# Performance work log

Measured on AMD Instinct MI355X. Metric: run time of the kernel, lower is better.

The kernel has to match this reference:

```python
import jax, jax.numpy as jnp
import numpy as np

C_IN = 96          # spectral bands
D2 = 2 * C_IN      # d = 192 (inner dim)
D4 = 4 * D2        # 768 (4-directional scan channels)
N = 16             # SSM state size
DR = 6             # delta_rank = ceil(96/16)
B, H, W = 2, 96, 96  # H,W not in {8,16,32,64} -> s=1 path


def setup_inputs() -> dict:
    key = jax.random.key(0)
    ks = jax.random.split(key, 8)
    g = lambda k, shape, s: jax.random.normal(k, shape, jnp.float32) * s
    return {
        "x": jax.random.normal(ks[0], (B, C_IN, H, W), jnp.float32),
        "W_in": g(ks[1], (C_IN, 2 * D2), 0.05),          # in_proj (in,out)
        "b_in": jnp.zeros((2 * D2,), jnp.float32),
        "w_dw": g(ks[2], (D2, 1, 3, 3), 0.1),            # depthwise conv OIHW
        "b_dw": jnp.zeros((D2,), jnp.float32),
        "A_log": jnp.log(jnp.tile(jnp.arange(1.0, N + 1.0, dtype=jnp.float32), (D4, 1))),
        "Dp": jnp.ones((D4,), jnp.float32),
        "W_x": g(ks[3], (D4, DR + 2 * N), 0.05),         # x_proj, no bias
        "W_delta": g(ks[4], (DR, D4), 0.1),
        "b_delta": g(ks[5], (D4,), 0.1),
        "ln_g": jnp.ones((D2,), jnp.float32),
        "ln_b": jnp.zeros((D2,), jnp.float32),
        "W_out": g(ks[6], (D2, C_IN), 0.05),             # out_proj, no bias
    }


def _selective_scan(u, delta, A, Bm, Cm, Dv):
    # u, delta: [b,L,d4]; Bm, Cm: [b,L,n]; A: [d4,n]; Dv: [d4]
    b, L, d4 = u.shape
    n = A.shape[1]

    def step(h, inps):
        u_t, dt, B_t, C_t = inps                      # [b,d4],[b,d4],[b,n],[b,n]
        dA = jnp.exp(dt[:, :, None] * A)              # [b,d4,n]
        h = dA * h + (dt * u_t)[:, :, None] * B_t[:, None, :]
        y = jnp.einsum('bdn,bn->bd', h, C_t) + Dv * u_t
        return h, y

    h0 = jnp.zeros((b, d4, n), u.dtype)
    xs = (jnp.swapaxes(u, 0, 1), jnp.swapaxes(delta, 0, 1),
          jnp.swapaxes(Bm, 0, 1), jnp.swapaxes(Cm, 0, 1))
    _, ys = jax.lax.scan(step, h0, xs)                # ys: [L,b,d4]
    return jnp.swapaxes(ys, 0, 1)                     # [b,L,d4]


def reference(x, W_in, b_in, w_dw, b_dw, A_log, Dp, W_x, W_delta, b_delta, ln_g, ln_b, W_out):
    b, c, Hh, Ww = x.shape                            # s = 1 (H not in {8,16,32,64})
    d = W_in.shape[1] // 2
    # in_proj on channel-last, chunk into x / gate z
    xz = jnp.einsum('bchw,ce->bhwe', x, W_in) + b_in  # [b,h,w,2d]
    xx, z = jnp.split(xz, 2, axis=-1)
    # depthwise conv + silu
    xc = jnp.transpose(xx, (0, 3, 1, 2))              # [b,d,h,w]
    xc = jax.lax.conv_general_dilated(
        xc, w_dw, (1, 1), 'SAME', feature_group_count=d,
        dimension_numbers=('NCHW', 'OIHW', 'NCHW')) + b_dw[None, :, None, None]
    xc = jax.nn.silu(xc)
    # 4 directional flattenings (with s=1: x1==x2 row-major, x3==x4 reversed)
    L = Hh * Ww
    flat = xc.reshape(b, d, L)
    flipped = xc[:, :, ::-1, ::-1].reshape(b, d, L)
    xl = jnp.swapaxes(jnp.concatenate([flat, flat, flipped, flipped], axis=1), 1, 2)  # [b,L,4d]
    # SSM parameterization
    A = -jnp.exp(A_log)                               # [4d,n]
    x_dbl = xl @ W_x                                  # [b,L,dr+2n]
    dr, n = W_delta.shape[0], A.shape[1]
    dt_r = x_dbl[..., :dr]
    Bm = x_dbl[..., dr:dr + n]
    Cm = x_dbl[..., dr + n:]
    delta = jax.nn.softplus(dt_r @ W_delta + b_delta)  # [b,L,4d]
    y = _selective_scan(xl, delta, A, Bm, Cm, Dp)      # [b,L,4d]
    # merge 4 directions back to spatial
    y = jnp.transpose(y.reshape(b, L, 4, d), (0, 2, 3, 1))  # [b,4,d,L]
    y1 = y[:, 0].reshape(b, d, Hh, Ww)
    y2 = y[:, 1].reshape(b, d, Hh, Ww)
    y3 = y[:, 2].reshape(b, d, Hh, Ww)[:, :, ::-1, ::-1]
    y4 = y[:, 3].reshape(b, d, Hh, Ww)[:, :, ::-1, ::-1]
    yh = jnp.transpose(y1 + y2 + y3 + y4, (0, 2, 3, 1))  # [b,h,w,d]
    # LayerNorm over d
    mu = yh.mean(-1, keepdims=True)
    var = ((yh - mu) ** 2).mean(-1, keepdims=True)
    yn = (yh - mu) * jax.lax.rsqrt(var + 1e-5) * ln_g + ln_b
    out = (yn * jax.nn.silu(z)) @ W_out               # [b,h,w,c]
    return jnp.transpose(out, (0, 3, 1, 2))           # [b,c,h,w]
```

## Files before the change

### kernel.cpp

```cpp
#include <hip/hip_runtime.h>
#include <hip/hip_bf16.h>
#include <math.h>

#define CIN 96
#define D2 192
#define D4 768
#define LL 9216
#define NN 16
#define NCH 288
#define CLEN 32

typedef float v2f __attribute__((ext_vector_type(2)));

#define SZ_Y4SLOT (2u*2u*9216u*192u)
#define SZ_BL    (2u*9216u*192u)
#define SZ_XDBL  (2u*9216u*38u)
#define SZ_S     (2u*4u*288u*192u)
#define SZ_HSLOT (2u*4u*288u*192u*8u)
#define F_Y4     0u
#define F_XX     0u
#define F_ZS     (F_Y4 + SZ_Y4SLOT)
#define F_XT     (F_ZS + SZ_BL)
#define F_XD0    (F_XT + SZ_BL)
#define F_XD1    (F_XD0 + SZ_XDBL)
#define F_XD2    (F_XD1 + SZ_XDBL)
#define F_XD3    (F_XD2 + SZ_XDBL)
#define F_SBUF   (F_XD3 + SZ_XDBL)
#define F_HBUF   (F_SBUF + SZ_S)
#define F_WCOMB  (F_HBUF + SZ_HSLOT)

__device__ __forceinline__ float silu_f(float z) {
    return z / (1.0f + __expf(-z));
}

__device__ __forceinline__ void pow_pairs(float e1, v2f p[8]) {
    float e2 = e1 * e1;
    v2f p01; p01.x = e1; p01.y = e2;
    v2f e2v; e2v.x = e2; e2v.y = e2;
    v2f e4v = e2v * e2v;
    v2f e8v = e4v * e4v;
    p[0] = p01;
    p[1] = p01 * e2v;
    p[2] = p01 * e4v;
    p[3] = p[1] * e4v;
    p[4] = p01 * e8v;
    p[5] = p[1] * e8v;
    p[6] = p[2] * e8v;
    p[7] = p[3] * e8v;
}

__global__ __launch_bounds__(256) void k0_foldw(
    const float* __restrict__ Wx, float* __restrict__ wcomb)
{
    int i = blockIdx.x * 256 + threadIdx.x;
    if (i >= 192 * 80) return;
    int d = i / 80, j = i % 80;
    float v = 0.f;
    if (j < 38) v = Wx[d * 38 + j] + Wx[(d + 192) * 38 + j];
    else if (j >= 40 && j < 78) {
        int jj = j - 40;
        v = Wx[(d + 384) * 38 + jj] + Wx[(d + 576) * 38 + jj];
    }
    wcomb[i] = v;
}

__global__ __launch_bounds__(256) void k1_inproj(
    const float* __restrict__ x, const float* __restrict__ Win,
    const float* __restrict__ bin, float* __restrict__ xx, float* __restrict__ zs)
{
    __shared__ float xs[96][36];
    __shared__ float wsh[96][68];
    int tid = threadIdx.x;
    int bid = blockIdx.x;
    int eh = bid & 1;
    int lt = bid >> 1;
    int gl0 = lt * 32;
    int b = gl0 / LL;
    int l0 = gl0 % LL;

    for (int i = tid; i < 96 * 32; i += 256) {
        int k = i >> 5, li = i & 31;
        xs[k][li] = x[(size_t)(b * 96 + k) * LL + l0 + li];
    }
    int lg = tid & 15;
    int eg = tid >> 4;
    for (int ch = 0; ch < 3; ch++) {
        int ecol0 = eh * 192 + ch * 64;
        __syncthreads();
        for (int i = tid; i < 96 * 64; i += 256) {
            int k = i >> 6, e = i & 63;
            wsh[k][e] = Win[k * 384 + ecol0 + e];
        }
        __syncthreads();
        v2f acc[4];
#pragma unroll
        for (int j = 0; j < 4; j++) { acc[j].x = 0.f; acc[j].y = 0.f; }
        for (int k = 0; k < 96; k++) {
            v2f x2 = *(const v2f*)&xs[k][lg * 2];
            float4 wv = *(const float4*)&wsh[k][eg * 4];
            float wa[4] = {wv.x, wv.y, wv.z, wv.w};
#pragma unroll
            for (int j = 0; j < 4; j++) {
                v2f wsp; wsp.x = wa[j]; wsp.y = wa[j];
                acc[j] += x2 * wsp;
            }
        }
        if (eh == 0) {
#pragma unroll
            for (int j = 0; j < 4; j++) {
                int e = ecol0 + eg * 4 + j;
                float bb = bin[e];
                float2 v = {acc[j].x + bb, acc[j].y + bb};
                *(float2*)&xx[(size_t)(b * 192 + e) * LL + l0 + lg * 2] = v;
            }
        } else {
            int rel0 = ch * 64 + eg * 4;
            float bb0 = bin[ecol0 + eg * 4 + 0];
            float bb1 = bin[ecol0 + eg * 4 + 1];
            float bb2 = bin[ecol0 + eg * 4 + 2];
            float bb3 = bin[ecol0 + eg * 4 + 3];
#pragma unroll
            for (int r = 0; r < 2; r++) {
                int l = l0 + lg * 2 + r;
                float4 v;
                v.x = silu_f(acc[0][r] + bb0);
                v.y = silu_f(acc[1][r] + bb1);
                v.z = silu_f(acc[2][r] + bb2);
                v.w = silu_f(acc[3][r] + bb3);
                *(float4*)&zs[((size_t)b * LL + l) * 192 + rel0] = v;
            }
        }
    }
}

__global__ __launch_bounds__(192) void k2_conv(
    const float* __restrict__ xx, const float* __restrict__ wdw,
    const float* __restrict__ bdw, float* __restrict__ xt)
{
    __shared__ float tile[32][97];
    __shared__ float wsm[32][9];
    __shared__ float bs[32];
    int tid = threadIdx.x;
    int bid = blockIdx.x;
    int h = bid % 96;
    int r = bid / 96;
    int dg = r % 6;
    int b = r / 6;

    for (int i = tid; i < 288; i += 192) wsm[i / 9][i % 9] = wdw[(dg * 32 + i / 9) * 9 + (i % 9)];
    if (tid < 32) bs[tid] = bdw[dg * 32 + tid];
    __syncthreads();

    int w = tid % 96;
    int dhalf = tid / 96;
    for (int p = 0; p < 16; p++) {
        int dsub = 2 * p + dhalf;
        const float* base = xx + (size_t)(b * 192 + dg * 32 + dsub) * LL;
        float acc = bs[dsub];
#pragma unroll
        for (int kh = 0; kh < 3; kh++) {
            int hh = h + kh - 1;
            if (hh < 0 || hh >= 96) continue;
            const float* row = base + hh * 96;
#pragma unroll
            for (int kw = 0; kw < 3; kw++) {
                int ww = w + kw - 1;
                if (ww < 0 || ww >= 96) continue;
                acc += row[ww] * wsm[dsub][kh * 3 + kw];
            }
        }
        tile[dsub][w] = silu_f(acc);
    }
    __syncthreads();
    for (int i = tid; i < 768; i += 192) {
        int q = i & 7, ls = i >> 3;
        float4 v = {tile[q * 4 + 0][ls], tile[q * 4 + 1][ls], tile[q * 4 + 2][ls], tile[q * 4 + 3][ls]};
        *(float4*)&xt[((size_t)b * LL + h * 96 + ls) * 192 + dg * 32 + q * 4] = v;
    }
}

__global__ __launch_bounds__(320) void k3_xdbl(
    const float* __restrict__ xt, const float* __restrict__ wcomb,
    float* __restrict__ xa0, float* __restrict__ xa1,
    float* __restrict__ xb0, float* __restrict__ xb1)
{
    __shared__ float xs[16][68];
    __shared__ float wsh[16][80];
    int tid = threadIdx.x;
    int bid = blockIdx.x;
    int kh = bid & 1;
    int rt = (bid >> 1) % 144;
    int b = bid / 288;
    int r0 = rt * 64;
    int k0 = kh * 96;
    float* __restrict__ xa = kh ? xa1 : xa0;
    float* __restrict__ xb = kh ? xb1 : xb0;

    int rg = tid / 20;
    int cg = tid % 20;
    v2f acc[4][2];
#pragma unroll
    for (int i = 0; i < 4; i++)
#pragma unroll
        for (int p = 0; p < 2; p++) { acc[i][p].x = 0.f; acc[i][p].y = 0.f; }

    for (int kc = 0; kc < 96; kc += 16) {
        __syncthreads();
        if (tid < 256) {
            int row = tid >> 2, dq = tid & 3;
            float4 v = *(const float4*)&xt[((size_t)b * LL + r0 + row) * 192 + k0 + kc + dq * 4];
            xs[dq * 4 + 0][row] = v.x;
            xs[dq * 4 + 1][row] = v.y;
            xs[dq * 4 + 2][row] = v.z;
            xs[dq * 4 + 3][row] = v.w;
        }
        for (int i = tid; i < 16 * 80; i += 320) {
            int d = i / 80, j = i - d * 80;
            wsh[d][j] = wcomb[(k0 + kc + d) * 80 + j];
        }
        __syncthreads();
#pragma unroll
        for (int d = 0; d < 16; d++) {
            float4 xv = *(const float4*)&xs[d][rg * 4];
            float4 wv = *(const float4*)&wsh[d][cg * 4];
            v2f w01; w01.x = wv.x; w01.y = wv.y;
            v2f w23; w23.x = wv.z; w23.y = wv.w;
            float xr[4] = {xv.x, xv.y, xv.z, xv.w};
#pragma unroll
            for (int i = 0; i < 4; i++) {
                v2f xi; xi.x = xr[i]; xi.y = xr[i];
                acc[i][0] += xi * w01;
                acc[i][1] += xi * w23;
            }
        }
    }
    int c0 = cg * 4;
#pragma unroll
    for (int i = 0; i < 4; i++) {
        int la = r0 + rg * 4 + i;
#pragma unroll
        for (int j = 0; j < 4; j++) {
            int col = c0 + j;
            float v = acc[i][j >> 1][j & 1];
            if (col < 38) {
                xa[((size_t)b * LL + la) * 38 + col] = v;
            } else if (col >= 40 && col < 78) {
                int lb = LL - 1 - la;
                xb[((size_t)b * LL + lb) * 38 + (col - 40)] = v;
            }
        }
    }
}

__global__ __launch_bounds__(192, 4) void k4_pass1(
    const float* __restrict__ xt,
    const float* __restrict__ xa0, const float* __restrict__ xa1,
    const float* __restrict__ xb0, const float* __restrict__ xb1,
    const float* __restrict__ Wd, const float* __restrict__ bdl,
    const float* __restrict__ Alog,
    float* __restrict__ Sbuf, __hip_bfloat16* __restrict__ Hbuf)
{
    __shared__ float Bt[CLEN][16];
    __shared__ float Dt[CLEN][6];
    int tid = threadIdx.x;
    int bid = blockIdx.x;
    int k = bid % NCH;
    int r = bid / NCH;
    int dir = r & 3;
    int b = r >> 2;
    int l0 = k * CLEN;
    for (int i = tid; i < CLEN * 16; i += 192) {
        int t = i >> 4, n = i & 15;
        size_t rb = ((size_t)b * LL + l0 + t) * 38 + 6 + n;
        Bt[t][n] = (xa0[rb] + xa1[rb]) + (xb0[rb] + xb1[rb]);
    }
    for (int i = tid; i < CLEN * 6; i += 192) {
        int t = i / 6, rr = i - 6 * t;
        size_t rb = ((size_t)b * LL + l0 + t) * 38 + rr;
        Dt[t][rr] = (xa0[rb] + xa1[rb]) + (xb0[rb] + xb1[rb]);
    }
    __syncthreads();
    int c = tid;
    int d4 = dir * 192 + c;
    float a0 = -__expf(Alog[d4 * 16]);
    bool fast = true;
    for (int n = 1; n < 16; n++) {
        float an = -__expf(Alog[d4 * 16 + n]);
        float tgt = (n + 1) * a0;
        fast = fast && (fabsf(an - tgt) <= 1e-5f * fabsf(tgt));
    }
    float wd[6];
#pragma unroll
    for (int rr = 0; rr < 6; rr++) wd[rr] = Wd[rr * 768 + d4];
    float bde = bdl[d4];
    float S = 0.f;
    const float* xtp = xt + (size_t)b * LL * 192 + c;
    int bd = b * 4 + dir;
    size_t base = (((size_t)bd * NCH + k) * 192 + c) * 16;
    if (fast) {
        v2f h2[8];
#pragma unroll
        for (int n = 0; n < 8; n++) { h2[n].x = 0.f; h2[n].y = 0.f; }
#pragma unroll 2
        for (int t = 0; t < CLEN; t++) {
            float s = bde;
#pragma unroll
            for (int rr = 0; rr < 6; rr++) s += Dt[t][rr] * wd[rr];
            float dt = (s > 20.f) ? s : __logf(1.f + __expf(s));
            S += dt;
            int lp = (dir < 2) ? (l0 + t) : (LL - 1 - (l0 + t));
            float u = xtp[(size_t)lp * 192];
            float du = dt * u;
            float4 q0 = *(const float4*)&Bt[t][0];
            float4 q1 = *(const float4*)&Bt[t][4];
            float4 q2 = *(const float4*)&Bt[t][8];
            float4 q3 = *(const float4*)&Bt[t][12];
            v2f B2[8];
            B2[0].x = q0.x; B2[0].y = q0.y; B2[1].x = q0.z; B2[1].y = q0.w;
            B2[2].x = q1.x; B2[2].y = q1.y; B2[3].x = q1.z; B2[3].y = q1.w;
            B2[4].x = q2.x; B2[4].y = q2.y; B2[5].x = q2.z; B2[5].y = q2.w;
            B2[6].x = q3.x; B2[6].y = q3.y; B2[7].x = q3.z; B2[7].y = q3.w;
            v2f p2[8];
            pow_pairs(__expf(dt * a0), p2);
            v2f du2; du2.x = du; du2.y = du;
#pragma unroll
            for (int n = 0; n < 8; n++) h2[n] = p2[n] * h2[n] + du2 * B2[n];
        }
        __hip_bfloat16* hb = Hbuf + base;
#pragma unroll
        for (int n = 0; n < 8; n++) {
            hb[2 * n]     = __float2bfloat16(h2[n].x);
            hb[2 * n + 1] = __float2bfloat16(h2[n].y);
        }
    } else {
        float h[16];
#pragma unroll
        for (int n = 0; n < 16; n++) h[n] = 0.f;
        for (int t = 0; t < CLEN; t++) {
            float s = bde;
#pragma unroll
            for (int rr = 0; rr < 6; rr++) s += Dt[t][rr] * wd[rr];
            float dt = (s > 20.f) ? s : __logf(1.f + __expf(s));
            S += dt;
            int lp = (dir < 2) ? (l0 + t) : (LL - 1 - (l0 + t));
            float u = xtp[(size_t)lp * 192];
            float du = dt * u;
#pragma unroll
            for (int n = 0; n < 16; n++) {
                float e = __expf(dt * (-__expf(Alog[d4 * 16 + n])));
                h[n] = e * h[n] + du * Bt[t][n];
            }
        }
#pragma unroll
        for (int n = 0; n < 16; n++) Hbuf[base + n] = __float2bfloat16(h[n]);
    }
    Sbuf[((size_t)bd * NCH + k) * 192 + c] = S;
}

__global__ __launch_bounds__(256) void k4_pass2(
    const float* __restrict__ Sbuf, const float* __restrict__ Alog,
    __hip_bfloat16* __restrict__ Hbuf)
{
    int lane = blockIdx.x * 256 + threadIdx.x;
    int bd = lane / 3072;
    int cn = lane % 3072;
    int c = cn >> 4, n = cn & 15;
    int dir = bd & 3;
    float an = -__expf(Alog[(dir * 192 + c) * 16 + n]);
    float h = 0.f;
#pragma unroll 8
    for (int k = 0; k < NCH; k++) {
        size_t sidx = ((size_t)bd * NCH + k) * 192 + c;
        float S = Sbuf[sidx];
        size_t idx = sidx * 16 + n;
        float hl = __bfloat162float(Hbuf[idx]);
        float P = __expf(an * S);
        Hbuf[idx] = __float2bfloat16(h);
        h = P * h + hl;
    }
}

__global__ __launch_bounds__(192, 4) void k4_pass3(
    const float* __restrict__ xt,
    const float* __restrict__ xa0, const float* __restrict__ xa1,
    const float* __restrict__ xb0, const float* __restrict__ xb1,
    const float* __restrict__ Wd, const float* __restrict__ bdl,
    const float* __restrict__ Alog, const float* __restrict__ Dp,
    const __hip_bfloat16* __restrict__ Hbuf, __hip_bfloat16* __restrict__ y4)
{
    __shared__ float Bt[CLEN][16];
    __shared__ float Ct[CLEN][16];
    __shared__ float Dt[CLEN][6];
    int tid = threadIdx.x;
    int bid = blockIdx.x;
    int k = bid % NCH;
    int r = bid / NCH;
    int dir = r & 3;
    int b = r >> 2;
    int l0 = k * CLEN;
    for (int i = tid; i < CLEN * 16; i += 192) {
        int t = i >> 4, n = i & 15;
        size_t rb = ((size_t)b * LL + l0 + t) * 38;
        size_t r1 = rb + 6 + n, r2 = rb + 22 + n;
        Bt[t][n] = (xa0[r1] + xa1[r1]) + (xb0[r1] + xb1[r1]);
        Ct[t][n] = (xa0[r2] + xa1[r2]) + (xb0[r2] + xb1[r2]);
    }
    for (int i = tid; i < CLEN * 6; i += 192) {
        int t = i / 6, rr = i - 6 * t;
        size_t rb = ((size_t)b * LL + l0 + t) * 38 + rr;
        Dt[t][rr] = (xa0[rb] + xa1[rb]) + (xb0[rb] + xb1[rb]);
    }
    __syncthreads();
    int c = tid;
    int d4 = dir * 192 + c;
    float a0 = -__expf(Alog[d4 * 16]);
    bool fast = true;
    for (int n = 1; n < 16; n++) {
        float an = -__expf(Alog[d4 * 16 + n]);
        float tgt = (n + 1) * a0;
        fast = fast && (fabsf(an - tgt) <= 1e-5f * fabsf(tgt));
    }
    float wd[6];
#pragma unroll
    for (int rr = 0; rr < 6; rr++) wd[rr] = Wd[rr * 768 + d4];
    float bde = bdl[d4];
    float Dv = Dp[d4];
    int bd = b * 4 + dir;
    size_t base = (((size_t)bd * NCH + k) * 192 + c) * 16;
    const float* xtp = xt + (size_t)b * LL * 192 + c;
    __hip_bfloat16* yp = y4 + (size_t)bd * LL * 192 + c;
    if (fast) {
        v2f h2[8];
        const __hip_bfloat16* hb = Hbuf + base;
#pragma unroll
        for (int n = 0; n < 8; n++) {
            h2[n].x = __bfloat162float(hb[2 * n]);
            h2[n].y = __bfloat162float(hb[2 * n + 1]);
        }
#pragma unroll 2
        for (int t = 0; t < CLEN; t++) {
            float s = bde;
#pragma unroll
            for (int rr = 0; rr < 6; rr++) s += Dt[t][rr] * wd[rr];
            float dt = (s > 20.f) ? s : __logf(1.f + __expf(s));
            int lp = (dir < 2) ? (l0 + t) : (LL - 1 - (l0 + t));
            float u = xtp[(size_t)lp * 192];
            float du = dt * u;
            float4 q0 = *(const float4*)&Bt[t][0];
            float4 q1 = *(const float4*)&Bt[t][4];
            float4 q2 = *(const float4*)&Bt[t][8];
            float4 q3 = *(const float4*)&Bt[t][12];
            v2f B2[8];
            B2[0].x = q0.x; B2[0].y = q0.y; B2[1].x = q0.z; B2[1].y = q0.w;
            B2[2].x = q1.x; B2[2].y = q1.y; B2[3].x = q1.z; B2[3].y = q1.w;
            B2[4].x = q2.x; B2[4].y = q2.y; B2[5].x = q2.z; B2[5].y = q2.w;
            B2[6].x = q3.x; B2[6].y = q3.y; B2[7].x = q3.z; B2[7].y = q3.w;
            float4 r0 = *(const float4*)&Ct[t][0];
            float4 r1 = *(const float4*)&Ct[t][4];
            float4 r2 = *(const float4*)&Ct[t][8];
            float4 r3 = *(const float4*)&Ct[t][12];
            v2f C2[8];
            C2[0].x = r0.x; C2[0].y = r0.y; C2[1].x = r0.z; C2[1].y = r0.w;
            C2[2].x = r1.x; C2[2].y = r1.y; C2[3].x = r1.z; C2[3].y = r1.w;
            C2[4].x = r2.x; C2[4].y = r2.y; C2[5].x = r2.z; C2[5].y = r2.w;
            C2[6].x = r3.x; C2[6].y = r3.y; C2[7].x = r3.z; C2[7].y = r3.w;
            v2f p2[8];
            pow_pairs(__expf(dt * a0), p2);
            v2f du2; du2.x = du; du2.y = du;
            v2f ya; ya.x = 0.f; ya.y = 0.f;
            v2f yb; yb.x = 0.f; yb.y = 0.f;
#pragma unroll
            for (int n = 0; n < 8; n += 2) {
                h2[n] = p2[n] * h2[n] + du2 * B2[n];
                ya += h2[n] * C2[n];
                h2[n + 1] = p2[n + 1] * h2[n + 1] + du2 * B2[n + 1];
                yb += h2[n + 1] * C2[n + 1];
            }
            float yv = (ya.x + ya.y) + (yb.x + yb.y) + Dv * u;
            yp[(size_t)lp * 192] = __float2bfloat16(yv);
        }
    } else {
        float h[16];
#pragma unroll
        for (int n = 0; n < 16; n++) h[n] = __bfloat162float(Hbuf[base + n]);
        for (int t = 0; t < CLEN; t++) {
            float s = bde;
#pragma unroll
            for (int rr = 0; rr < 6; rr++) s += Dt[t][rr] * wd[rr];
            float dt = (s > 20.f) ? s : __logf(1.f + __expf(s));
            int lp = (dir < 2) ? (l0 + t) : (LL - 1 - (l0 + t));
            float u = xtp[(size_t)lp * 192];
            float du = dt * u;
            float yv = Dv * u;
#pragma unroll
            for (int n = 0; n < 16; n++) {
                float e = __expf(dt * (-__expf(Alog[d4 * 16 + n])));
                h[n] = e * h[n] + du * Bt[t][n];
                yv += h[n] * Ct[t][n];
            }
            yp[(size_t)lp * 192] = __float2bfloat16(yv);
        }
    }
}

__global__ __launch_bounds__(256) void k5_out(
    const __hip_bfloat16* __restrict__ y4, const float* __restrict__ zs,
    const float* __restrict__ lng, const float* __restrict__ lnb,
    const float* __restrict__ Wout, float* __restrict__ out)
{
    __shared__ float acts[16][196];
    __shared__ float wsh[16][100];
    int tid = threadIdx.x;
    int wv = tid >> 6;
    int lane = tid & 63;
    int gl0 = blockIdx.x * 16;
    int b = gl0 / LL;
    int l0 = gl0 % LL;
    const size_t ds = (size_t)LL * 192;

    for (int i = 0; i < 4; i++) {
        int rrow = wv * 4 + i;
        int l = l0 + rrow;
        float yv[3], zv[3];
        float s1 = 0.f, s2 = 0.f;
#pragma unroll
        for (int kk = 0; kk < 3; kk++) {
            int c = lane + kk * 64;
            size_t off = ((size_t)(b * 4) * LL + l) * 192 + c;
            float y = __bfloat162float(y4[off]) + __bfloat162float(y4[off + ds])
                    + __bfloat162float(y4[off + 2 * ds]) + __bfloat162float(y4[off + 3 * ds]);
            yv[kk] = y;
            zv[kk] = zs[((size_t)b * LL + l) * 192 + c];
            s1 += y; s2 += y * y;
        }
#pragma unroll
        for (int o = 32; o; o >>= 1) {
            s1 += __shfl_xor(s1, o, 64);
            s2 += __shfl_xor(s2, o, 64);
        }
        float mean = s1 * (1.f / 192.f);
        float var = s2 * (1.f / 192.f) - mean * mean;
        float rs = rsqrtf(var + 1e-5f);
#pragma unroll
        for (int kk = 0; kk < 3; kk++) {
            int c = lane + kk * 64;
            float yn = (yv[kk] - mean) * rs * lng[c] + lnb[c];
            acts[rrow][c] = yn * zv[kk];
        }
    }

    int ty = tid & 15;
    int tx = tid >> 4;
    v2f o2[3];
    o2[0].x = 0.f; o2[0].y = 0.f;
    o2[1].x = 0.f; o2[1].y = 0.f;
    o2[2].x = 0.f; o2[2].y = 0.f;

    for (int kc = 0; kc < 192; kc += 16) {
        __syncthreads();
        for (int i = tid; i < 16 * 96; i += 256) {
            int d = i / 96, j = i - d * 96;
            wsh[d][j] = Wout[(kc + d) * 96 + j];
        }
        __syncthreads();
#pragma unroll
        for (int kk = 0; kk < 16; kk++) {
            float av = acts[ty][kc + kk];
            const v2f* wp = (const v2f*)&wsh[kk][tx * 6];
            v2f w0 = wp[0], w1 = wp[1], w2 = wp[2];
            v2f sp; sp.x = av; sp.y = av;
            o2[0] += sp * w0;
            o2[1] += sp * w1;
            o2[2] += sp * w2;
        }
    }
    int l = l0 + ty;
#pragma unroll
    for (int j = 0; j < 6; j++) {
        int n = tx * 6 + j;
        out[((size_t)(b * 96) + n) * LL + l] = o2[j >> 1][j & 1];
    }
}

extern "C" void kernel_launch(void* const* d_in, const int* in_sizes, int n_in,
                              void* d_out, int out_size, void* d_ws, size_t ws_size,
                              hipStream_t stream)
{
    const float* x    = (const float*)d_in[0];
    const float* Win  = (const float*)d_in[1];
    const float* bin  = (const float*)d_in[2];
    const float* wdw  = (const float*)d_in[3];
    const float* bdw  = (const float*)d_in[4];
    const float* Alog = (const float*)d_in[5];
    const float* Dp   = (const float*)d_in[6];
    const float* Wx   = (const float*)d_in[7];
    const float* Wd   = (const float*)d_in[8];
    const float* bdl  = (const float*)d_in[9];
    const float* lng  = (const float*)d_in[10];
    const float* lnb  = (const float*)d_in[11];
    const float* Wout = (const float*)d_in[12];
    float* out = (float*)d_out;

    float* ws    = (float*)d_ws;
    __hip_bfloat16* y4 = (__hip_bfloat16*)(ws + F_Y4);
    float* xx    = ws + F_XX;
    float* zs    = ws + F_ZS;
    float* xt    = ws + F_XT;
    float* xd0   = ws + F_XD0;
    float* xd1   = ws + F_XD1;
    float* xd2   = ws + F_XD2;
    float* xd3   = ws + F_XD3;
    float* Sbuf  = ws + F_SBUF;
    __hip_bfloat16* Hbuf = (__hip_bfloat16*)(ws + F_HBUF);
    float* wcomb = ws + F_WCOMB;

    k0_foldw<<<60, 256, 0, stream>>>(Wx, wcomb);
    k1_inproj<<<1152, 256, 0, stream>>>(x, Win, bin, xx, zs);
    k2_conv<<<1152, 192, 0, stream>>>(xx, wdw, bdw, xt);
    k3_xdbl<<<576, 320, 0, stream>>>(xt, wcomb, xd0, xd1, xd2, xd3);
    k4_pass1<<<2304, 192, 0, stream>>>(xt, xd0, xd1, xd2, xd3, Wd, bdl, Alog, Sbuf, Hbuf);
    k4_pass2<<<96, 256, 0, stream>>>(Sbuf, Alog, Hbuf);
    k4_pass3<<<2304, 192, 0, stream>>>(xt, xd0, xd1, xd2, xd3, Wd, bdl, Alog, Dp, Hbuf, y4);
    k5_out<<<1152, 256, 0, stream>>>(y4, zs, lng, lnb, Wout, out);
}
```

Measured before the change: 306.5 us.

## Precompute A fast-path flags, restructure scan power chain, widen out-proj weight tiles

Measured after the change: 294.1 us. 4.0% less time.

```diff
diff --git a/kernel.cpp b/kernel.cpp
--- a/kernel.cpp
+++ b/kernel.cpp
@@ -28,31 +28,29 @@
 #define F_SBUF   (F_XD3 + SZ_XDBL)
 #define F_HBUF   (F_SBUF + SZ_S)
 #define F_WCOMB  (F_HBUF + SZ_HSLOT)
+#define F_A0     (F_WCOMB + 15360u)
+#define F_FF     (F_A0 + 768u)
 
 __device__ __forceinline__ float silu_f(float z) {
     return z / (1.0f + __expf(-z));
 }
 
-__device__ __forceinline__ void pow_pairs(float e1, v2f p[8]) {
-    float e2 = e1 * e1;
-    v2f p01; p01.x = e1; p01.y = e2;
-    v2f e2v; e2v.x = e2; e2v.y = e2;
-    v2f e4v = e2v * e2v;
-    v2f e8v = e4v * e4v;
-    p[0] = p01;
-    p[1] = p01 * e2v;
-    p[2] = p01 * e4v;
-    p[3] = p[1] * e4v;
-    p[4] = p01 * e8v;
-    p[5] = p[1] * e8v;
-    p[6] = p[2] * e8v;
-    p[7] = p[3] * e8v;
-}
-
 __global__ __launch_bounds__(256) void k0_foldw(
-    const float* __restrict__ Wx, float* __restrict__ wcomb)
+    const float* __restrict__ Wx, const float* __restrict__ Alog,
+    float* __restrict__ wcomb, float* __restrict__ A0f, float* __restrict__ Ffl)
 {
     int i = blockIdx.x * 256 + threadIdx.x;
+    if (i < 768) {
+        float a0 = -__expf(Alog[i * 16]);
+        bool fast = true;
+        for (int n = 1; n < 16; n++) {
+            float an = -__expf(Alog[i * 16 + n]);
+            float tgt = (n + 1) * a0;
+            fast = fast && (fabsf(an - tgt) <= 1e-5f * fabsf(tgt));
+        }
+        A0f[i] = a0;
+        Ffl[i] = fast ? 1.f : 0.f;
+    }
     if (i >= 192 * 80) return;
     int d = i / 80, j = i % 80;
     float v = 0.f;
@@ -257,7 +255,8 @@
     const float* __restrict__ xa0, const float* __restrict__ xa1,
     const float* __restrict__ xb0, const float* __restrict__ xb1,
     const float* __restrict__ Wd, const float* __restrict__ bdl,
-    const float* __restrict__ Alog,
+    const float* __restrict__ Alog, const float* __restrict__ A0f,
+    const float* __restrict__ Ffl,
     float* __restrict__ Sbuf, __hip_bfloat16* __restrict__ Hbuf)
 {
     __shared__ float Bt[CLEN][16];
@@ -282,13 +281,8 @@
     __syncthreads();
     int c = tid;
     int d4 = dir * 192 + c;
-    float a0 = -__expf(Alog[d4 * 16]);
-    bool fast = true;
-    for (int n = 1; n < 16; n++) {
-        float an = -__expf(Alog[d4 * 16 + n]);
-        float tgt = (n + 1) * a0;
-        fast = fast && (fabsf(an - tgt) <= 1e-5f * fabsf(tgt));
-    }
+    float a0 = A0f[d4];
+    bool fast = (Ffl[d4] != 0.f);
     float wd[6];
 #pragma unroll
     for (int rr = 0; rr < 6; rr++) wd[rr] = Wd[rr * 768 + d4];
@@ -303,28 +297,32 @@
         for (int n = 0; n < 8; n++) { h2[n].x = 0.f; h2[n].y = 0.f; }
 #pragma unroll 2
         for (int t = 0; t < CLEN; t++) {
-            float s = bde;
-#pragma unroll
-            for (int rr = 0; rr < 6; rr++) s += Dt[t][rr] * wd[rr];
+            float2 d01 = *(const float2*)&Dt[t][0];
+            float2 d23 = *(const float2*)&Dt[t][2];
+            float2 d45 = *(const float2*)&Dt[t][4];
+            float s = bde + d01.x * wd[0] + d01.y * wd[1] + d23.x * wd[2]
+                          + d23.y * wd[3] + d45.x * wd[4] + d45.y * wd[5];
             float dt = (s > 20.f) ? s : __logf(1.f + __expf(s));
             S += dt;
             int lp = (dir < 2) ? (l0 + t) : (LL - 1 - (l0 + t));
             float u = xtp[(size_t)lp * 192];
             float du = dt * u;
-            float4 q0 = *(const float4*)&Bt[t][0];
-            float4 q1 = *(const float4*)&Bt[t][4];
-            float4 q2 = *(const float4*)&Bt[t][8];
-            float4 q3 = *(const float4*)&Bt[t][12];
-            v2f B2[8];
-            B2[0].x = q0.x; B2[0].y = q0.y; B2[1].x = q0.z; B2[1].y = q0.w;
-            B2[2].x = q1.x; B2[2].y = q1.y; B2[3].x = q1.z; B2[3].y = q1.w;
-            B2[4].x = q2.x; B2[4].y = q2.y; B2[5].x = q2.z; B2[5].y = q2.w;
-            B2[6].x = q3.x; B2[6].y = q3.y; B2[7].x = q3.z; B2[7].y = q3.w;
-            v2f p2[8];
-            pow_pairs(__expf(dt * a0), p2);
+            float e1 = __expf(dt * a0);
+            float e2 = e1 * e1;
+            v2f q; q.x = e1; q.y = e2;
+            v2f e2v; e2v.x = e2; e2v.y = e2;
+            v2f e4v = e2v * e2v;
+            v2f q2 = q * e2v;
             v2f du2; du2.x = du; du2.y = du;
 #pragma unroll
-            for (int n = 0; n < 8; n++) h2[n] = p2[n] * h2[n] + du2 * B2[n];
+            for (int g = 0; g < 4; g++) {
+                float4 bq = *(const float4*)&Bt[t][4 * g];
+                v2f b0; b0.x = bq.x; b0.y = bq.y;
+                v2f b1; b1.x = bq.z; b1.y = bq.w;
+                h2[2 * g]     = q  * h2[2 * g]     + du2 * b0;
+                h2[2 * g + 1] = q2 * h2[2 * g + 1] + du2 * b1;
+                if (g < 3) { q *= e4v; q2 *= e4v; }
+            }
         }
         __hip_bfloat16* hb = Hbuf + base;
 #pragma unroll
@@ -385,7 +383,8 @@
     const float* __restrict__ xa0, const float* __restrict__ xa1,
     const float* __restrict__ xb0, const float* __restrict__ xb1,
     const float* __restrict__ Wd, const float* __restrict__ bdl,
-    const float* __restrict__ Alog, const float* __restrict__ Dp,
+    const float* __restrict__ Alog, const float* __restrict__ A0f,
+    const float* __restrict__ Ffl, const float* __restrict__ Dp,
     const __hip_bfloat16* __restrict__ Hbuf, __hip_bfloat16* __restrict__ y4)
 {
     __shared__ float Bt[CLEN][16];
@@ -413,13 +412,8 @@
     __syncthreads();
     int c = tid;
     int d4 = dir * 192 + c;
-    float a0 = -__expf(Alog[d4 * 16]);
-    bool fast = true;
-    for (int n = 1; n < 16; n++) {
-        float an = -__expf(Alog[d4 * 16 + n]);
-        float tgt = (n + 1) * a0;
-        fast = fast && (fabsf(an - tgt) <= 1e-5f * fabsf(tgt));
-    }
+    float a0 = A0f[d4];
+    bool fast = (Ffl[d4] != 0.f);
     float wd[6];
 #pragma unroll
     for (int rr = 0; rr < 6; rr++) wd[rr] = Wd[rr * 768 + d4];
@@ -439,42 +433,37 @@
         }
 #pragma unroll 2
         for (int t = 0; t < CLEN; t++) {
-            float s = bde;
-#pragma unroll
-            for (int rr = 0; rr < 6; rr++) s += Dt[t][rr] * wd[rr];
+            float2 d01 = *(const float2*)&Dt[t][0];
+            float2 d23 = *(const float2*)&Dt[t][2];
+            float2 d45 = *(const float2*)&Dt[t][4];
+            float s = bde + d01.x * wd[0] + d01.y * wd[1] + d23.x * wd[2]
+                          + d23.y * wd[3] + d45.x * wd[4] + d45.y * wd[5];
             float dt = (s > 20.f) ? s : __logf(1.f + __expf(s));
             int lp = (dir < 2) ? (l0 + t) : (LL - 1 - (l0 + t));
             float u = xtp[(size_t)lp * 192];
             float du = dt * u;
-            float4 q0 = *(const float4*)&Bt[t][0];
-            float4 q1 = *(const float4*)&Bt[t][4];
-            float4 q2 = *(const float4*)&Bt[t][8];
-            float4 q3 = *(const float4*)&Bt[t][12];
-            v2f B2[8];
-            B2[0].x = q0.x; B2[0].y = q0.y; B2[1].x = q0.z; B2[1].y = q0.w;
-            B2[2].x = q1.x; B2[2].y = q1.y; B2[3].x = q1.z; B2[3].y = q1.w;
-            B2[4].x = q2.x; B2[4].y = q2.y; B2[5].x = q2.z; B2[5].y = q2.w;
-            B2[6].x = q3.x; B2[6].y = q3.y; B2[7].x = q3.z; B2[7].y = q3.w;
-            float4 r0 = *(const float4*)&Ct[t][0];
-            float4 r1 = *(const float4*)&Ct[t][4];
-            float4 r2 = *(const float4*)&Ct[t][8];
-            float4 r3 = *(const float4*)&Ct[t][12];
-            v2f C2[8];
-            C2[0].x = r0.x; C2[0].y = r0.y; C2[1].x = r0.z; C2[1].y = r0.w;
-            C2[2].x = r1.x; C2[2].y = r1.y; C2[3].x = r1.z; C2[3].y = r1.w;
-            C2[4].x = r2.x; C2[4].y = r2.y; C2[5].x = r2.z; C2[5].y = r2.w;
-            C2[6].x = r3.x; C2[6].y = r3.y; C2[7].x = r3.z; C2[7].y = r3.w;
-            v2f p2[8];
-            pow_pairs(__expf(dt * a0), p2);
+            float e1 = __expf(dt * a0);
+            float e2 = e1 * e1;
+            v2f q; q.x = e1; q.y = e2;
+            v2f e2v; e2v.x = e2; e2v.y = e2;
+            v2f e4v = e2v * e2v;
+            v2f q2 = q * e2v;
             v2f du2; du2.x = du; du2.y = du;
             v2f ya; ya.x = 0.f; ya.y = 0.f;
             v2f yb; yb.x = 0.f; yb.y = 0.f;
 #pragma unroll
-            for (int n = 0; n < 8; n += 2) {
-                h2[n] = p2[n] * h2[n] + du2 * B2[n];
-                ya += h2[n] * C2[n];
-                h2[n + 1] = p2[n + 1] * h2[n + 1] + du2 * B2[n + 1];
-                yb += h2[n + 1] * C2[n + 1];
+            for (int g = 0; g < 4; g++) {
+                float4 bq = *(const float4*)&Bt[t][4 * g];
+                float4 cq = *(const float4*)&Ct[t][4 * g];
+                v2f b0; b0.x = bq.x; b0.y = bq.y;
+                v2f b1; b1.x = bq.z; b1.y = bq.w;
+                v2f c0v; c0v.x = cq.x; c0v.y = cq.y;
+                v2f c1v; c1v.x = cq.z; c1v.y = cq.w;
+                h2[2 * g]     = q  * h2[2 * g]     + du2 * b0;
+                ya += h2[2 * g] * c0v;
+                h2[2 * g + 1] = q2 * h2[2 * g + 1] + du2 * b1;
+                yb += h2[2 * g + 1] * c1v;
+                if (g < 3) { q *= e4v; q2 *= e4v; }
             }
             float yv = (ya.x + ya.y) + (yb.x + yb.y) + Dv * u;
             yp[(size_t)lp * 192] = __float2bfloat16(yv);
@@ -509,7 +498,7 @@
     const float* __restrict__ Wout, float* __restrict__ out)
 {
     __shared__ float acts[16][196];
-    __shared__ float wsh[16][100];
+    __shared__ float wsh[32][100];
     int tid = threadIdx.x;
     int wv = tid >> 6;
     int lane = tid & 63;
@@ -556,15 +545,15 @@
     o2[1].x = 0.f; o2[1].y = 0.f;
     o2[2].x = 0.f; o2[2].y = 0.f;
 
-    for (int kc = 0; kc < 192; kc += 16) {
+    for (int kc = 0; kc < 192; kc += 32) {
         __syncthreads();
-        for (int i = tid; i < 16 * 96; i += 256) {
-            int d = i / 96, j = i - d * 96;
-            wsh[d][j] = Wout[(kc + d) * 96 + j];
+        for (int i = tid; i < 32 * 24; i += 256) {
+            int d = i / 24, q = i - d * 24;
+            *(float4*)&wsh[d][q * 4] = *(const float4*)&Wout[(kc + d) * 96 + q * 4];
         }
         __syncthreads();
 #pragma unroll
-        for (int kk = 0; kk < 16; kk++) {
+        for (int kk = 0; kk < 32; kk++) {
             float av = acts[ty][kc + kk];
             const v2f* wp = (const v2f*)&wsh[kk][tx * 6];
             v2f w0 = wp[0], w1 = wp[1], w2 = wp[2];
@@ -613,13 +602,15 @@
     float* Sbuf  = ws + F_SBUF;
     __hip_bfloat16* Hbuf = (__hip_bfloat16*)(ws + F_HBUF);
     float* wcomb = ws + F_WCOMB;
-
-    k0_foldw<<<60, 256, 0, stream>>>(Wx, wcomb);
+    float* A0f   = ws + F_A0;
+    float* Ffl   = ws + F_FF;
+
+    k0_foldw<<<60, 256, 0, stream>>>(Wx, Alog, wcomb, A0f, Ffl);
     k1_inproj<<<1152, 256, 0, stream>>>(x, Win, bin, xx, zs);
     k2_conv<<<1152, 192, 0, stream>>>(xx, wdw, bdw, xt);
     k3_xdbl<<<576, 320, 0, stream>>>(xt, wcomb, xd0, xd1, xd2, xd3);
-    k4_pass1<<<2304, 192, 0, stream>>>(xt, xd0, xd1, xd2, xd3, Wd, bdl, Alog, Sbuf, Hbuf);
+    k4_pass1<<<2304, 192, 0, stream>>>(xt, xd0, xd1, xd2, xd3, Wd, bdl, Alog, A0f, Ffl, Sbuf, Hbuf);
     k4_pass2<<<96, 256, 0, stream>>>(Sbuf, Alog, Hbuf);
-    k4_pass3<<<2304, 192, 0, stream>>>(xt, xd0, xd1, xd2, xd3, Wd, bdl, Alog, Dp, Hbuf, y4);
+    k4_pass3<<<2304, 192, 0, stream>>>(xt, xd0, xd1, xd2, xd3, Wd, bdl, Alog, A0f, Ffl, Dp, Hbuf, y4);
     k5_out<<<1152, 256, 0, stream>>>(y4, zs, lng, lnb, Wout, out);
 }
```
